# Performance work log

Measured on AMD Instinct MI355X. Metric: run time of the kernel, lower is better.

The kernel has to match this reference:

```python
import jax, jax.numpy as jnp
import numpy as np

PS = 7        # pooled_size == conved_size
IMG = 300     # img_size
FMAP = 19     # feature map spatial size
SMAX = IMG // 16  # clamp max (18), matches torch long clamp(0, 300/16)
EPS = 1e-5


def _bn(x, g, b, m, v):
    scale = (g * jax.lax.rsqrt(v + EPS))[None, :, None, None]
    return x * scale + (b - m * g * jax.lax.rsqrt(v + EPS))[None, :, None, None]


def _conv(x, W, b=None, pad=1):
    y = jax.lax.conv_general_dilated(x, W, (1, 1), [(pad, pad), (pad, pad)],
                                     dimension_numbers=('NCHW', 'OIHW', 'NCHW'))
    if b is not None:
        y = y + b[None, :, None, None]
    return y


def _adaptive_w(lo, hi):
    # Per-ROI adaptive-avg-pool weights over the full 19-wide axis.
    # lo, hi: [B,R] inclusive crop bounds. Returns [B,R,PS,FMAP].
    H = hi - lo + 1                                  # crop length per ROI
    i = jnp.arange(PS)
    s = (i[None, None, :] * H[..., None]) // PS      # bin start (floor)
    e = -((-(i[None, None, :] + 1) * H[..., None]) // PS)  # bin end (ceil)
    rows = jnp.arange(FMAP)
    start = lo[..., None, None] + s[..., None]
    stop = lo[..., None, None] + e[..., None]
    mask = (rows >= start) & (rows < stop)
    denom = jnp.maximum(e - s, 1).astype(jnp.float32)[..., None]
    return mask.astype(jnp.float32) / denom


def setup_inputs() -> dict:
    key = jax.random.key(0)
    ks = jax.random.split(key, 6)
    B, R = 8, 128
    return {
        'roi_proposal': jax.random.uniform(ks[0], (B, 1, R, 5), dtype=jnp.float32),
        'features': jax.random.normal(ks[1], (B, 1024, FMAP, FMAP), dtype=jnp.float32),
        'W1': jax.random.normal(ks[2], (256, 1024, 3, 3), dtype=jnp.float32) * 0.02,
        'b1': jnp.zeros((256,), jnp.float32),
        'g1': jnp.ones((256,), jnp.float32),
        'be1': jnp.zeros((256,), jnp.float32),
        'm1': jnp.zeros((256,), jnp.float32),
        'v1': jnp.ones((256,), jnp.float32),
        'W2': jax.random.normal(ks[3], (256, 256, 3, 3), jnp.float32) * 0.05,
        'b2': jnp.zeros((256,), jnp.float32),
        'g2': jnp.ones((256,), jnp.float32),
        'be2': jnp.zeros((256,), jnp.float32),
        'm2': jnp.zeros((256,), jnp.float32),
        'v2': jnp.ones((256,), jnp.float32),
        'W3': jax.random.normal(ks[4], (32, 256, 1, 1), jnp.float32) * 0.1,
        'g3': jnp.ones((32,), jnp.float32),
        'be3': jnp.zeros((32,), jnp.float32),
        'm3': jnp.zeros((32,), jnp.float32),
        'v3': jnp.ones((32,), jnp.float32),
    }


def reference(roi_proposal, features, W1, b1, g1, be1, m1, v1,
              W2, b2, g2, be2, m2, v2, W3, g3, be3, m3, v3):
    # rois[..., 1:] * img_size / 16, then trunc to long (coords are >= 0)
    rl = (roi_proposal[:, 0, :, 1:] * (IMG / 16.0)).astype(jnp.int32)  # [B,R,4]
    c = jnp.clip(rl, 0, SMAX)
    xmin, ymin, xmax, ymax = c[..., 0], c[..., 1], c[..., 2], c[..., 3]
    valid = (xmax > xmin) & (ymax > ymin)                              # [B,R]
    B, R = valid.shape

    # fused crop + adaptive avg pool as two small pooling matmuls per ROI
    Wy = _adaptive_w(ymin, ymax)   # [B,R,7,19]
    Wx = _adaptive_w(xmin, xmax)   # [B,R,7,19]
    pooled = jnp.einsum('brph,bchw,brqw->brcpq', Wy, features, Wx)     # [B,R,1024,7,7]

    x = pooled.reshape(B * R, 1024, PS, PS)
    x = jax.nn.relu(_bn(_conv(x, W1, b1), g1, be1, m1, v1))
    x = jax.nn.relu(_bn(_conv(x, W2, b2), g2, be2, m2, v2))
    x = jax.nn.relu(_bn(_conv(x, W3, None, pad=0), g3, be3, m3, v3))
    out = x.reshape(B, R, 32, PS, PS) * valid[:, :, None, None, None]

    # compact valid ROIs to the front per batch (stable), invalid slots zeroed
    perm = jnp.argsort((~valid).astype(jnp.int32), axis=1, stable=True)
    out_c = jax.vmap(lambda o, p: o[p])(out, perm)                     # [B,R,32,7,7]
    er = rl.astype(jnp.float32) * (16.0 / IMG) * valid[..., None]
    er_c = jax.vmap(lambda o, p: o[p])(er, perm)[:, None]              # [B,1,R,4]
    keep_count = valid.sum(axis=1).astype(jnp.int32)                   # [B]
    return er_c, out_c, keep_count
```

## Files before the change

### kernel.cpp

```cpp
#include <hip/hip_runtime.h>
#include <cstddef>
#include <cstdint>

typedef unsigned short u16;
typedef unsigned int u32;
typedef __attribute__((ext_vector_type(8))) short short8;
typedef __attribute__((ext_vector_type(4))) float f32x4;

#define NB 8
#define NR 128
#define NPOS 49
#define EPSV 1e-5f
#define NSLOT 512

#define OUT_OC   4096
#define OUT_KEEP 1609728

static constexpr size_t OFF_META = 256;
static constexpr size_t OFF_KEEP = 33024;
static constexpr size_t OFF_W1Q  = 40960;
static constexpr size_t OFF_W2Q  = OFF_W1Q + 4718592;
static constexpr size_t OFF_W3   = OFF_W2Q + 1179648;
static constexpr size_t OFF_X1S  = OFF_W3  + 32768;
static constexpr size_t OFF_AP   = OFF_X1S + 13107200;
static constexpr size_t WS_NEED  = OFF_AP  + 51380224;

static __device__ __forceinline__ u16 f2bf(float f) {
  union { float f; u32 u; } x; x.f = f;
  u32 r = 0x7fffu + ((x.u >> 16) & 1u);
  return (u16)((x.u + r) >> 16);
}

__device__ __forceinline__ void int_body(const float* __restrict__ feat, float* __restrict__ S,
                                         int b, int cg, float* F)
{
  int tid = threadIdx.x;
  const float* fb = feat + ((size_t)b * 1024 + cg * 64) * 361;
#pragma unroll 1
  for (int i = tid; i < 64 * 361; i += 256) F[i] = fb[i];
  __syncthreads();
  if (tid < 64) {
    int ch = tid;
    const float* fp = F + ch * 361;
    float* Sp = S + (size_t)b * 400 * 1024 + cg * 64 + ch;
    float prev[20];
#pragma unroll
    for (int w = 0; w < 20; ++w) { prev[w] = 0.f; Sp[(size_t)w * 1024] = 0.f; }
    for (int h = 0; h < 19; ++h) {
      float run = 0.f;
      float* Sr = Sp + (size_t)(h + 1) * 20 * 1024;
      Sr[0] = 0.f;
#pragma unroll
      for (int w = 0; w < 19; ++w) {
        run += fp[h * 19 + w];
        float v = run + prev[w + 1];
        Sr[(size_t)(w + 1) * 1024] = v;
        prev[w + 1] = v;
      }
    }
  }
}

__device__ __forceinline__ void packw_body(const float* __restrict__ W, u16* __restrict__ wq,
                                           int IC, int c, int og, float* F)
{
  int tid = threadIdx.x, oc0 = og * 32;
#pragma unroll 1
  for (int i = tid; i < 18432; i += 256) {
    int ocr = i / 576, r = i - ocr * 576;
    F[i] = W[(size_t)(oc0 + ocr) * IC * 9 + c * 576 + r];
  }
  __syncthreads();
#pragma unroll 1
  for (int w = tid; w < 18432; w += 256) {
    int j = w & 7, lane = (w >> 3) & 63, rest = w >> 9;
    int ntr = rest & 1, kk = rest >> 1;
    int k9i = kk >> 1, ks = kk & 1;
    int ocr = ntr * 16 + (lane & 15);
    int icr = ks * 32 + ((lane >> 4) & 3) * 8 + j;
    int bid_ = (c * 9 + k9i) * 2 + ks;
    wq[((size_t)bid_ * 1024 + (oc0 / 16 + ntr) * 64 + lane) * 8 + j] = f2bf(F[ocr * 576 + icr * 9 + k9i]);
  }
}

__global__ __launch_bounds__(256) void k_prep(
    const float* __restrict__ feat, float* __restrict__ S,
    const float* __restrict__ W1, const float* __restrict__ W2, const float* __restrict__ W3,
    u16* __restrict__ w1q, u16* __restrict__ w2q, u16* __restrict__ w3q,
    const float* __restrict__ roi, int* __restrict__ cnt,
    int* __restrict__ meta, int* __restrict__ keepd, float* __restrict__ out)
{
  __shared__ float SH[23104];
  int bx = blockIdx.x;
  if (bx < 128) { int_body(feat, S, bx >> 4, bx & 15, SH); return; }
  if (bx < 256) { packw_body(W1, w1q, 1024, (bx - 128) >> 3, (bx - 128) & 7, SH); return; }
  if (bx < 288) { packw_body(W2, w2q, 256, (bx - 256) >> 3, (bx - 256) & 7, SH); return; }
  if (bx == 288) {
    for (int i = threadIdx.x; i < 8192; i += 256) {
      int oc = i >> 8, ic = i & 255;
      int kk = ic >> 5;
      int lane = ((ic >> 3) & 3) * 16 + (oc & 15);
      int nt16 = oc >> 4;
      int j = ic & 7;
      w3q[((size_t)((kk * 2 + nt16) * 64) + lane) * 8 + j] = f2bf(W3[i]);
    }
    return;
  }
  int b = bx - 289, t = threadIdx.x;
  int* sval = (int*)SH;
  int* spre = sval + 128;
  int rl[4], cl[4], valid = 0;
  if (t < 128) {
    const float* rp = roi + (size_t)(b * NR + t) * 5;
#pragma unroll
    for (int j = 0; j < 4; ++j) {
      rl[j] = (int)(rp[1 + j] * 18.75f);
      cl[j] = min(max(rl[j], 0), 18);
    }
    valid = (cl[2] > cl[0]) && (cl[3] > cl[1]) ? 1 : 0;
    sval[t] = valid;
  }
  __syncthreads();
  if (t == 0) {
    int s = 0;
    for (int i = 0; i < 128; ++i) { spre[i] = s; s += sval[i]; }
    spre[128] = s;
    keepd[b] = s;
    out[OUT_KEEP + b] = (float)s;
  }
  __syncthreads();
  if (t < 128) {
    int keep = spre[128];
    if (valid) {
      int dst = spre[t];
      int slot = atomicAdd(cnt, 1);
      int* mt = meta + slot * 8;
      mt[0] = b; mt[1] = dst;
      mt[2] = cl[1]; mt[3] = cl[3];
      mt[4] = cl[0]; mt[5] = cl[2];
#pragma unroll
      for (int j = 0; j < 4; ++j)
        out[(size_t)(b * NR + dst) * 4 + j] = (float)rl[j] * (16.0f / 300.0f);
    }
    if (t >= keep) {
#pragma unroll
      for (int j = 0; j < 4; ++j) out[(size_t)(b * NR + t) * 4 + j] = 0.f;
    }
  }
}

__global__ __launch_bounds__(256) void k_pool(
    const int* __restrict__ cnt, const int* __restrict__ meta,
    const float* __restrict__ S, u16* __restrict__ Apool)
{
  int cv = *cnt; if (cv > NSLOT) cv = NSLOT;
  int slot = blockIdx.x;
  if (slot >= cv) return;
  const int* mt_ = meta + slot * 8;
  int b = mt_[0], ylo = mt_[2], yhi = mt_[3], xlo = mt_[4], xhi = mt_[5];
  int Hy = yhi - ylo + 1, Hx = xhi - xlo + 1;
  const float* Sb = S + (size_t)b * 400 * 1024;
  u16* Ap = Apool + (size_t)slot * 50176;
  int base = blockIdx.y * 12544, end = base + 12544;
  int tid = threadIdx.x;
#pragma unroll 1
  for (int t0 = base + tid; t0 < end; t0 += 1024) {
#pragma unroll
    for (int u = 0; u < 4; ++u) {
      int t = t0 + u * 256;
      if (t < end) {
        int ch = t & 63, r = t >> 6;
        int bin = r % 49, c = r / 49;
        int p = bin / 7, q = bin - 7 * p;
        int sy = (p * Hy) / 7, ey = ((p + 1) * Hy + 6) / 7;
        int sx = (q * Hx) / 7, ex = ((q + 1) * Hx + 6) / 7;
        int y0 = ylo + sy, y1 = ylo + ey, x0 = xlo + sx, x1 = xlo + ex;
        const float* Sc = Sb + c * 64 + ch;
        float v = Sc[(size_t)(y1 * 20 + x1) * 1024] - Sc[(size_t)(y0 * 20 + x1) * 1024]
                - Sc[(size_t)(y1 * 20 + x0) * 1024] + Sc[(size_t)(y0 * 20 + x0) * 1024];
        v /= (float)((ey - sy) * (ex - sx));
        Ap[(size_t)c * 3136 + bin * 64 + ch] = f2bf(v);
      }
    }
  }
}

template<int STR>
__device__ __forceinline__ void build_aoffp(int n, int kq, int (&aoffp)[9][2]) {
#pragma unroll
  for (int t9 = 0; t9 < 9; ++t9) {
    int off[4];
#pragma unroll
    for (int mt = 0; mt < 4; ++mt) {
      int lm = mt * 16 + n;
      int mv = lm < 49;
      int lm2 = mv ? lm : 0;
      int p = lm2 / 7, q = lm2 - 7 * p;
      int ky = t9 / 3, kx = t9 - 3 * (t9 / 3);
      int ry = p + ky - 1, rx = q + kx - 1;
      int ok = mv && ry >= 0 && ry < 7 && rx >= 0 && rx < 7;
      int rr = ok ? ry * 7 + rx : 49;
      off[mt] = rr * STR + kq * 8;
    }
    aoffp[t9][0] = (off[0] & 0xFFFF) | (off[1] << 16);
    aoffp[t9][1] = (off[2] & 0xFFFF) | (off[3] << 16);
  }
}

__global__ __launch_bounds__(1024) void k_conv1(
    const int* __restrict__ cnt, const u16* __restrict__ Apool, const u16* __restrict__ wq,
    const float* __restrict__ bb, const float* __restrict__ gg, const float* __restrict__ bec,
    const float* __restrict__ mm, const float* __restrict__ vv,
    u16* __restrict__ x1)
{
  int cv = *cnt; if (cv > NSLOT) cv = NSLOT;
  int slot0 = blockIdx.x * 4, ocq = blockIdx.y;
  if (slot0 >= cv) return;

  __shared__ __align__(16) u16 panels[8 * 3600];
  float* red = (float*)panels;

  int tid = threadIdx.x, lane = tid & 63, wave = tid >> 6;
  int roi4 = wave & 3, och = (wave >> 2) & 1, kh = wave >> 3;
  int n = lane & 15, kq = lane >> 4;

  for (int i = tid; i < 8 * 36; i += 1024) {
    int sp = i / 36, w2 = i - sp * 36;
    ((u32*)(panels + sp * 3600 + 49 * 72))[w2] = 0;
  }

  int aoffp[9][2];
  build_aoffp<72>(n, kq, aoffp);
  f32x4 acc[4][2];
#pragma unroll
  for (int i = 0; i < 4; ++i)
#pragma unroll
    for (int j = 0; j < 2; ++j) acc[i][j] = (f32x4){0.f, 0.f, 0.f, 0.f};

  const u16* pf = wq + (size_t)(ocq * 4 + och * 2) * 512 + (size_t)lane * 8
                + (size_t)(kh * 8) * 18 * 8192;
  short8 bbuf[2][2];
#pragma unroll
  for (int nt = 0; nt < 2; ++nt) bbuf[0][nt] = *(const short8*)(pf + nt * 512);
#pragma unroll
  for (int nt = 0; nt < 2; ++nt) bbuf[1][nt] = *(const short8*)(pf + 8192 + nt * 512);
  pf += (size_t)2 * 8192;

  auto stage = [&](int ca, int cb) {
#pragma unroll 1
    for (int t = tid; t < 3136; t += 1024) {
      int khs = t >= 1568 ? 1 : 0;
      int e2 = t - khs * 1568;
      int rr = e2 / 392, e = e2 - rr * 392;
      int c = khs ? cb : ca;
      int sl = slot0 + rr; if (sl >= cv) sl = cv - 1;
      uint4 v = *((const uint4*)(Apool + ((size_t)sl * 16 + c) * 3136) + e);
      *(uint4*)(panels + (size_t)(khs * 4 + rr) * 3600 + (e >> 3) * 72 + (e & 7) * 8) = v;
    }
  };

  stage(0, 8);
  __syncthreads();

  const u16* P = panels + (size_t)(kh * 4 + roi4) * 3600;
#pragma unroll 1
  for (int i = 0; i < 8; ++i) {
#pragma unroll
    for (int kk = 0; kk < 18; ++kk) {
      int t9 = kk >> 1, ks = kk & 1;
      short8 bfr[2], afr[4];
#pragma unroll
      for (int nt = 0; nt < 2; ++nt) bfr[nt] = bbuf[kk & 1][nt];
#pragma unroll
      for (int nt = 0; nt < 2; ++nt) bbuf[kk & 1][nt] = *(const short8*)(pf + nt * 512);
      pf += 8192;
      int coff = ks * 32;
      int o0 = (aoffp[t9][0] & 0xFFFF) + coff, o1 = (int)((u32)aoffp[t9][0] >> 16) + coff;
      int o2 = (aoffp[t9][1] & 0xFFFF) + coff, o3 = (int)((u32)aoffp[t9][1] >> 16) + coff;
      afr[0] = *(const short8*)(P + o0); afr[1] = *(const short8*)(P + o1);
      afr[2] = *(const short8*)(P + o2); afr[3] = *(const short8*)(P + o3);
#pragma unroll
      for (int mt = 0; mt < 4; ++mt)
#pragma unroll
        for (int nt = 0; nt < 2; ++nt)
          acc[mt][nt] = __builtin_amdgcn_mfma_f32_16x16x32_bf16(afr[mt], bfr[nt], acc[mt][nt], 0, 0, 0);
    }
    __syncthreads();
    if (i + 1 < 8) {
      stage(i + 1, 9 + i);
      __syncthreads();
    }
  }

  if (kh == 1) {
#pragma unroll
    for (int nt = 0; nt < 2; ++nt)
#pragma unroll
      for (int mt = 0; mt < 4; ++mt)
#pragma unroll
        for (int r = 0; r < 4; ++r) {
          int m = mt * 16 + kq * 4 + r;
          if (m < 49) red[(((size_t)roi4 * 2 + och) * 49 + m) * 32 + nt * 16 + n] = acc[mt][nt][r];
        }
  }
  __syncthreads();
  if (kh == 0) {
    int slot = slot0 + roi4;
    if (slot < cv) {
#pragma unroll
      for (int nt = 0; nt < 2; ++nt) {
        int oc = ocq * 64 + och * 32 + nt * 16 + n;
        float sc = gg[oc] * rsqrtf(vv[oc] + EPSV);
        float sh = (bb[oc] - mm[oc]) * sc + bec[oc];
#pragma unroll
        for (int mt = 0; mt < 4; ++mt)
#pragma unroll
          for (int r = 0; r < 4; ++r) {
            int m = mt * 16 + kq * 4 + r;
            if (m < 49) {
              float y = acc[mt][nt][r] + red[(((size_t)roi4 * 2 + och) * 49 + m) * 32 + nt * 16 + n];
              y = fmaf(y, sc, sh);
              x1[((size_t)slot * 4 + ocq) * 3136 + m * 64 + (oc & 63)] = f2bf(y > 0.f ? y : 0.f);
            }
          }
      }
    }
  }
}

__global__ __launch_bounds__(1024) void k_conv23(
    const int* __restrict__ cnt, const int* __restrict__ meta, const int* __restrict__ keepd,
    const u16* __restrict__ x1, const u16* __restrict__ w2q, const u16* __restrict__ w3q,
    const float* __restrict__ b2, const float* __restrict__ g2, const float* __restrict__ be2,
    const float* __restrict__ m2, const float* __restrict__ v2,
    const float* __restrict__ g3, const float* __restrict__ be3,
    const float* __restrict__ m3, const float* __restrict__ v3,
    float* __restrict__ out)
{
  int cv = *cnt; if (cv > NSLOT) cv = NSLOT;
  int slot = blockIdx.x;
  int tid = threadIdx.x;
  if (slot >= cv) {
    int nfill = NSLOT - cv;
#pragma unroll 1
    for (int j = slot - cv; j < 1024; j += nfill) {
      int b = j >> 7, dd = j & 127;
      if (dd >= keepd[b]) {
        float* o = out + OUT_OC + (size_t)(b * NR + dd) * 1568;
        for (int t = tid; t < 1568; t += 1024) o[t] = 0.f;
      }
    }
    return;
  }
  const int* mt_ = meta + slot * 8;
  int b = mt_[0], dst = mt_[1];

  __shared__ __align__(16) char smem[77600];
  u16*   panels = (u16*)smem;
  float* red    = (float*)smem;
  u16*   xp     = (u16*)(smem + 51200);
  float* red3   = (float*)smem;

  int lane = tid & 63, wave = tid >> 6;
  int ng = wave & 7, kh = wave >> 3;
  int n = lane & 15, kq = lane >> 4;

  for (int i = tid; i < 4 * 36; i += 1024) {
    int sp = i / 36, w2 = i - sp * 36;
    ((u32*)(panels + sp * 3600 + 49 * 72))[w2] = 0;
  }
  const u16* xs = x1 + (size_t)slot * 4 * 3136;
#pragma unroll 1
  for (int t = tid; t < 1568; t += 1024) {
    int c = t / 392, e = t - c * 392;
    uint4 v = *((const uint4*)(xs + (size_t)c * 3136) + e);
    *(uint4*)(panels + (size_t)c * 3600 + (e >> 3) * 72 + (e & 7) * 8) = v;
  }

  int aoffp[9][2];
  build_aoffp<72>(n, kq, aoffp);
  f32x4 acc[4][2];
#pragma unroll
  for (int i = 0; i < 4; ++i)
#pragma unroll
    for (int j = 0; j < 2; ++j) acc[i][j] = (f32x4){0.f, 0.f, 0.f, 0.f};

  const u16* pf = w2q + (size_t)(ng * 2) * 512 + (size_t)lane * 8 + (size_t)(kh * 36) * 8192;
  short8 bbuf[2][2];
#pragma unroll
  for (int nt = 0; nt < 2; ++nt) bbuf[0][nt] = *(const short8*)(pf + nt * 512);
#pragma unroll
  for (int nt = 0; nt < 2; ++nt) bbuf[1][nt] = *(const short8*)(pf + 8192 + nt * 512);
  pf += (size_t)2 * 8192;

  __syncthreads();

#pragma unroll 1
  for (int ci = 0; ci < 2; ++ci) {
    const u16* P = panels + (size_t)(kh * 2 + ci) * 3600;
#pragma unroll
    for (int kk = 0; kk < 18; ++kk) {
      int t9 = kk >> 1, ks = kk & 1;
      short8 bfr[2], afr[4];
#pragma unroll
      for (int nt = 0; nt < 2; ++nt) bfr[nt] = bbuf[kk & 1][nt];
#pragma unroll
      for (int nt = 0; nt < 2; ++nt) bbuf[kk & 1][nt] = *(const short8*)(pf + nt * 512);
      pf += 8192;
      int coff = ks * 32;
      int o0 = (aoffp[t9][0] & 0xFFFF) + coff, o1 = (int)((u32)aoffp[t9][0] >> 16) + coff;
      int o2 = (aoffp[t9][1] & 0xFFFF) + coff, o3 = (int)((u32)aoffp[t9][1] >> 16) + coff;
      afr[0] = *(const short8*)(P + o0); afr[1] = *(const short8*)(P + o1);
      afr[2] = *(const short8*)(P + o2); afr[3] = *(const short8*)(P + o3);
#pragma unroll
      for (int mt = 0; mt < 4; ++mt)
#pragma unroll
        for (int nt = 0; nt < 2; ++nt)
          acc[mt][nt] = __builtin_amdgcn_mfma_f32_16x16x32_bf16(afr[mt], bfr[nt], acc[mt][nt], 0, 0, 0);
    }
  }
  __syncthreads();

  if (kh == 1) {
#pragma unroll
    for (int nt = 0; nt < 2; ++nt)
#pragma unroll
      for (int mt = 0; mt < 4; ++mt)
#pragma unroll
        for (int r = 0; r < 4; ++r) {
          int m = mt * 16 + kq * 4 + r;
          if (m < 49) red[((size_t)ng * 49 + m) * 32 + nt * 16 + n] = acc[mt][nt][r];
        }
  }
  __syncthreads();
  if (kh == 0) {
#pragma unroll
    for (int nt = 0; nt < 2; ++nt) {
      int oc = ng * 32 + nt * 16 + n;
      float sc = g2[oc] * rsqrtf(v2[oc] + EPSV);
      float sh = (b2[oc] - m2[oc]) * sc + be2[oc];
#pragma unroll
      for (int mt = 0; mt < 4; ++mt)
#pragma unroll
        for (int r = 0; r < 4; ++r) {
          int m = mt * 16 + kq * 4 + r;
          if (m < 49) {
            float y = acc[mt][nt][r] + red[((size_t)ng * 49 + m) * 32 + nt * 16 + n];
            y = fmaf(y, sc, sh);
            xp[m * 264 + oc] = f2bf(y > 0.f ? y : 0.f);
          }
        }
    }
  }
  if (wave == 8) {
    for (int i = lane; i < 132; i += 64) ((u32*)(xp + 49 * 264))[i] = 0;
  }
  __syncthreads();

  if (wave < 8) {
    f32x4 a3[4][2];
#pragma unroll
    for (int mt = 0; mt < 4; ++mt) { a3[mt][0] = (f32x4){0,0,0,0}; a3[mt][1] = (f32x4){0,0,0,0}; }
    const u16* b3 = w3q + ((size_t)(wave * 2) * 64 + lane) * 8;
    short8 bf0 = *(const short8*)(b3);
    short8 bf1 = *(const short8*)(b3 + 512);
#pragma unroll
    for (int mt = 0; mt < 4; ++mt) {
      int m = mt * 16 + n;
      int row = m < 49 ? m : 49;
      short8 a = *(const short8*)(xp + row * 264 + wave * 32 + kq * 8);
      a3[mt][0] = __builtin_amdgcn_mfma_f32_16x16x32_bf16(a, bf0, a3[mt][0], 0, 0, 0);
      a3[mt][1] = __builtin_amdgcn_mfma_f32_16x16x32_bf16(a, bf1, a3[mt][1], 0, 0, 0);
    }
#pragma unroll
    for (int nt = 0; nt < 2; ++nt)
#pragma unroll
      for (int mt = 0; mt < 4; ++mt)
#pragma unroll
        for (int r = 0; r < 4; ++r) {
          int m = mt * 16 + kq * 4 + r;
          if (m < 49) red3[((size_t)wave * 49 + m) * 32 + nt * 16 + n] = a3[mt][nt][r];
        }
  }
  __syncthreads();

  size_t ob = OUT_OC + ((size_t)(b * NR + dst) * 32) * 49;
#pragma unroll 1
  for (int t = tid; t < 1568; t += 1024) {
    int m = t >> 5, oc = t & 31;
    float s = 0.f;
#pragma unroll
    for (int w8 = 0; w8 < 8; ++w8) s += red3[((size_t)w8 * 49 + m) * 32 + oc];
    float sc = g3[oc] * rsqrtf(v3[oc] + EPSV);
    float y = fmaf(s, sc, be3[oc] - m3[oc] * sc);
    out[ob + (size_t)oc * 49 + m] = y > 0.f ? y : 0.f;
  }
}

extern "C" void kernel_launch(void* const* d_in, const int* in_sizes, int n_in,
                              void* d_out, int out_size, void* d_ws, size_t ws_size,
                              hipStream_t stream)
{
  (void)in_sizes; (void)n_in; (void)out_size;
  if (ws_size < WS_NEED) return;

  const float* roi  = (const float*)d_in[0];
  const float* feat = (const float*)d_in[1];
  const float* W1   = (const float*)d_in[2];
  const float* b1   = (const float*)d_in[3];
  const float* g1   = (const float*)d_in[4];
  const float* be1  = (const float*)d_in[5];
  const float* m1   = (const float*)d_in[6];
  const float* v1   = (const float*)d_in[7];
  const float* W2   = (const float*)d_in[8];
  const float* b2   = (const float*)d_in[9];
  const float* g2   = (const float*)d_in[10];
  const float* be2  = (const float*)d_in[11];
  const float* m2   = (const float*)d_in[12];
  const float* v2   = (const float*)d_in[13];
  const float* W3   = (const float*)d_in[14];
  const float* g3   = (const float*)d_in[15];
  const float* be3  = (const float*)d_in[16];
  const float* m3   = (const float*)d_in[17];
  const float* v3   = (const float*)d_in[18];

  char* ws    = (char*)d_ws;
  int*  cnt   = (int*)ws;
  int*  meta  = (int*)(ws + OFF_META);
  int*  keepd = (int*)(ws + OFF_KEEP);
  u16*  w1q   = (u16*)(ws + OFF_W1Q);
  u16*  w2q   = (u16*)(ws + OFF_W2Q);
  u16*  w3q   = (u16*)(ws + OFF_W3);
  float* S    = (float*)(ws + OFF_X1S);
  u16*  x1    = (u16*)(ws + OFF_X1S);
  u16*  Apool = (u16*)(ws + OFF_AP);
  float* out  = (float*)d_out;

  hipMemsetAsync(cnt, 0, 4, stream);

  k_prep<<<297, 256, 0, stream>>>(feat, S, W1, W2, W3, w1q, w2q, w3q,
                                  roi, cnt, meta, keepd, out);
  k_pool<<<dim3(NSLOT, 4), 256, 0, stream>>>(cnt, meta, S, Apool);
  k_conv1<<<dim3(NSLOT / 4, 4), 1024, 0, stream>>>(cnt, Apool, w1q, b1, g1, be1, m1, v1, x1);
  k_conv23<<<NSLOT, 1024, 0, stream>>>(cnt, meta, keepd, x1, w2q, w3q,
                                       b2, g2, be2, m2, v2, g3, be3, m3, v3, out);
}
```

Baseline: 271.7 us.

## Restructure conv1 waves: full 64-channel tiles with three-way K split

conv1 now runs 12 waves (768 threads) instead of 16. Each wave computes all 64 output channels of its ROI (4 N-tiles, up from 2), and the 16 input-channel groups are split three ways (6/5/5) instead of two ways. The aim is to reuse each A fragment across twice as many MFMAs and to cut redundant LDS A-reads. The cost is more accumulator and B-buffer registers, uneven work across the K splits, a larger shared buffer for the two partial-sum reductions, and more stage rounds.

```diff
diff --git a/kernel.cpp b/kernel.cpp
--- a/kernel.cpp
+++ b/kernel.cpp
@@ -207,7 +207,7 @@
   }
 }
 
-__global__ __launch_bounds__(1024) void k_conv1(
+__global__ __launch_bounds__(768) void k_conv1(
     const int* __restrict__ cnt, const u16* __restrict__ Apool, const u16* __restrict__ wq,
     const float* __restrict__ bb, const float* __restrict__ gg, const float* __restrict__ bec,
     const float* __restrict__ mm, const float* __restrict__ vv,
@@ -217,90 +217,98 @@
   int slot0 = blockIdx.x * 4, ocq = blockIdx.y;
   if (slot0 >= cv) return;
 
-  __shared__ __align__(16) u16 panels[8 * 3600];
-  float* red = (float*)panels;
+  __shared__ __align__(16) char smem[100352];
+  u16* panels = (u16*)smem;
+  float* red1 = (float*)smem;
+  float* red2 = (float*)(smem + 50176);
 
   int tid = threadIdx.x, lane = tid & 63, wave = tid >> 6;
-  int roi4 = wave & 3, och = (wave >> 2) & 1, kh = wave >> 3;
+  int roi4 = wave & 3, kh = wave >> 2;
   int n = lane & 15, kq = lane >> 4;
-
-  for (int i = tid; i < 8 * 36; i += 1024) {
+  const int cbase = (kh == 0) ? 0 : (kh == 1 ? 6 : 11);
+  const int ccnt  = (kh == 0) ? 6 : 5;
+
+  for (int i = tid; i < 12 * 36; i += 768) {
     int sp = i / 36, w2 = i - sp * 36;
     ((u32*)(panels + sp * 3600 + 49 * 72))[w2] = 0;
   }
 
   int aoffp[9][2];
   build_aoffp<72>(n, kq, aoffp);
-  f32x4 acc[4][2];
+  f32x4 acc[4][4];
 #pragma unroll
   for (int i = 0; i < 4; ++i)
 #pragma unroll
-    for (int j = 0; j < 2; ++j) acc[i][j] = (f32x4){0.f, 0.f, 0.f, 0.f};
-
-  const u16* pf = wq + (size_t)(ocq * 4 + och * 2) * 512 + (size_t)lane * 8
-                + (size_t)(kh * 8) * 18 * 8192;
-  short8 bbuf[2][2];
-#pragma unroll
-  for (int nt = 0; nt < 2; ++nt) bbuf[0][nt] = *(const short8*)(pf + nt * 512);
-#pragma unroll
-  for (int nt = 0; nt < 2; ++nt) bbuf[1][nt] = *(const short8*)(pf + 8192 + nt * 512);
+    for (int j = 0; j < 4; ++j) acc[i][j] = (f32x4){0.f, 0.f, 0.f, 0.f};
+
+  const u16* pf = wq + (size_t)(ocq * 4) * 512 + (size_t)lane * 8 + (size_t)cbase * 18 * 8192;
+  short8 bbuf[2][4];
+#pragma unroll
+  for (int nt = 0; nt < 4; ++nt) bbuf[0][nt] = *(const short8*)(pf + nt * 512);
+#pragma unroll
+  for (int nt = 0; nt < 4; ++nt) bbuf[1][nt] = *(const short8*)(pf + 8192 + nt * 512);
   pf += (size_t)2 * 8192;
 
-  auto stage = [&](int ca, int cb) {
-#pragma unroll 1
-    for (int t = tid; t < 3136; t += 1024) {
-      int khs = t >= 1568 ? 1 : 0;
-      int e2 = t - khs * 1568;
+  auto stage = [&](int nr) {
+#pragma unroll 1
+    for (int t = tid; t < 4704; t += 768) {
+      int kh3 = t / 1568, e2 = t - kh3 * 1568;
       int rr = e2 / 392, e = e2 - rr * 392;
-      int c = khs ? cb : ca;
-      int sl = slot0 + rr; if (sl >= cv) sl = cv - 1;
-      uint4 v = *((const uint4*)(Apool + ((size_t)sl * 16 + c) * 3136) + e);
-      *(uint4*)(panels + (size_t)(khs * 4 + rr) * 3600 + (e >> 3) * 72 + (e & 7) * 8) = v;
+      int cn = (kh3 == 0) ? 6 : 5;
+      if (nr < cn) {
+        int c = ((kh3 == 0) ? 0 : (kh3 == 1 ? 6 : 11)) + nr;
+        int sl = slot0 + rr; if (sl >= cv) sl = cv - 1;
+        uint4 v = *((const uint4*)(Apool + ((size_t)sl * 16 + c) * 3136) + e);
+        *(uint4*)(panels + (size_t)(kh3 * 4 + rr) * 3600 + (e >> 3) * 72 + (e & 7) * 8) = v;
+      }
     }
   };
 
-  stage(0, 8);
+  stage(0);
   __syncthreads();
 
   const u16* P = panels + (size_t)(kh * 4 + roi4) * 3600;
 #pragma unroll 1
-  for (int i = 0; i < 8; ++i) {
-#pragma unroll
-    for (int kk = 0; kk < 18; ++kk) {
-      int t9 = kk >> 1, ks = kk & 1;
-      short8 bfr[2], afr[4];
-#pragma unroll
-      for (int nt = 0; nt < 2; ++nt) bfr[nt] = bbuf[kk & 1][nt];
-#pragma unroll
-      for (int nt = 0; nt < 2; ++nt) bbuf[kk & 1][nt] = *(const short8*)(pf + nt * 512);
-      pf += 8192;
-      int coff = ks * 32;
-      int o0 = (aoffp[t9][0] & 0xFFFF) + coff, o1 = (int)((u32)aoffp[t9][0] >> 16) + coff;
-      int o2 = (aoffp[t9][1] & 0xFFFF) + coff, o3 = (int)((u32)aoffp[t9][1] >> 16) + coff;
-      afr[0] = *(const short8*)(P + o0); afr[1] = *(const short8*)(P + o1);
-      afr[2] = *(const short8*)(P + o2); afr[3] = *(const short8*)(P + o3);
-#pragma unroll
-      for (int mt = 0; mt < 4; ++mt)
-#pragma unroll
-        for (int nt = 0; nt < 2; ++nt)
-          acc[mt][nt] = __builtin_amdgcn_mfma_f32_16x16x32_bf16(afr[mt], bfr[nt], acc[mt][nt], 0, 0, 0);
+  for (int r = 0; r < 6; ++r) {
+    if (r < ccnt) {
+#pragma unroll
+      for (int kk = 0; kk < 18; ++kk) {
+        int t9 = kk >> 1, ks = kk & 1;
+        short8 bfr[4], afr[4];
+#pragma unroll
+        for (int nt = 0; nt < 4; ++nt) bfr[nt] = bbuf[kk & 1][nt];
+#pragma unroll
+        for (int nt = 0; nt < 4; ++nt) bbuf[kk & 1][nt] = *(const short8*)(pf + nt * 512);
+        pf += 8192;
+        int coff = ks * 32;
+        int o0 = (aoffp[t9][0] & 0xFFFF) + coff, o1 = (int)((u32)aoffp[t9][0] >> 16) + coff;
+        int o2 = (aoffp[t9][1] & 0xFFFF) + coff, o3 = (int)((u32)aoffp[t9][1] >> 16) + coff;
+        afr[0] = *(const short8*)(P + o0); afr[1] = *(const short8*)(P + o1);
+        afr[2] = *(const short8*)(P + o2); afr[3] = *(const short8*)(P + o3);
+#pragma unroll
+        for (int mt = 0; mt < 4; ++mt)
+#pragma unroll
+          for (int nt = 0; nt < 4; ++nt)
+            acc[mt][nt] = __builtin_amdgcn_mfma_f32_16x16x32_bf16(afr[mt], bfr[nt], acc[mt][nt], 0, 0, 0);
+      }
     }
     __syncthreads();
-    if (i + 1 < 8) {
-      stage(i + 1, 9 + i);
+    if (r + 1 < 6) {
+      stage(r + 1);
       __syncthreads();
     }
   }
 
-  if (kh == 1) {
-#pragma unroll
-    for (int nt = 0; nt < 2; ++nt)
+  if (kh == 1 || kh == 2) {
+    float* rd = (kh == 1) ? red1 : red2;
+#pragma unroll
+    for (int nt = 0; nt < 4; ++nt)
 #pragma unroll
       for (int mt = 0; mt < 4; ++mt)
 #pragma unroll
         for (int r = 0; r < 4; ++r) {
           int m = mt * 16 + kq * 4 + r;
-          if (m < 49) red[(((size_t)roi4 * 2 + och) * 49 + m) * 32 + nt * 16 + n] = acc[mt][nt][r];
+          if (m < 49) rd[((size_t)roi4 * 49 + m) * 64 + nt * 16 + n] = acc[mt][nt][r];
         }
   }
   __syncthreads();
@@ -308,8 +316,8 @@
     int slot = slot0 + roi4;
     if (slot < cv) {
 #pragma unroll
-      for (int nt = 0; nt < 2; ++nt) {
-        int oc = ocq * 64 + och * 32 + nt * 16 + n;
+      for (int nt = 0; nt < 4; ++nt) {
+        int oc = ocq * 64 + nt * 16 + n;
         float sc = gg[oc] * rsqrtf(vv[oc] + EPSV);
         float sh = (bb[oc] - mm[oc]) * sc + bec[oc];
 #pragma unroll
@@ -318,7 +326,8 @@
           for (int r = 0; r < 4; ++r) {
             int m = mt * 16 + kq * 4 + r;
             if (m < 49) {
-              float y = acc[mt][nt][r] + red[(((size_t)roi4 * 2 + och) * 49 + m) * 32 + nt * 16 + n];
+              size_t ix = ((size_t)roi4 * 49 + m) * 64 + nt * 16 + n;
+              float y = acc[mt][nt][r] + red1[ix] + red2[ix];
               y = fmaf(y, sc, sh);
               x1[((size_t)slot * 4 + ocq) * 3136 + m * 64 + (oc & 63)] = f2bf(y > 0.f ? y : 0.f);
             }
@@ -541,7 +550,7 @@
   k_prep<<<297, 256, 0, stream>>>(feat, S, W1, W2, W3, w1q, w2q, w3q,
                                   roi, cnt, meta, keepd, out);
   k_pool<<<dim3(NSLOT, 4), 256, 0, stream>>>(cnt, meta, S, Apool);
-  k_conv1<<<dim3(NSLOT / 4, 4), 1024, 0, stream>>>(cnt, Apool, w1q, b1, g1, be1, m1, v1, x1);
+  k_conv1<<<dim3(NSLOT / 4, 4), 768, 0, stream>>>(cnt, Apool, w1q, b1, g1, be1, m1, v1, x1);
   k_conv23<<<NSLOT, 1024, 0, stream>>>(cnt, meta, keepd, x1, w2q, w3q,
                                        b2, g2, be2, m2, v2, g3, be3, m3, v3, out);
 }
```

New measurement: 276.4 us. Within noise of the previous version (+1.7%).
